# Kernel optimization log

Measured on AMD Instinct MI355X. Metric: run time of the kernel, lower is better.

Reference implementation:

```python
import jax, jax.numpy as jnp
import numpy as np

B, S_SRC, S_TRG = 128, 512, 128
VIN, VOUT = 128, 128
E, H = 128, 256          # embed, encoder hidden
HD = 2 * H               # decoder hidden = 512 (concat of bi-dir encoder states)
DENC = 2 * H             # encoder output feature dim = 512


def setup_inputs() -> dict:
    key = jax.random.key(0)
    ks = jax.random.split(key, 20)
    g = lambda k, shape: (jax.random.normal(k, shape, jnp.float32) * 0.05)
    inp = {
        "src": jax.random.randint(ks[0], (B, S_SRC), 0, VIN, jnp.int32),
        "trg": jax.random.randint(ks[1], (B, S_TRG), 0, VOUT, jnp.int32),
        # encoder
        "enc_emb": g(ks[2], (VIN, E)),
        "enc_Wih_f": g(ks[3], (4 * H, E)),
        "enc_Whh_f": g(ks[4], (4 * H, H)),
        "enc_b_f": g(ks[5], (4 * H,)),
        "enc_Wih_b": g(ks[6], (4 * H, E)),
        "enc_Whh_b": g(ks[7], (4 * H, H)),
        "enc_b_b": g(ks[8], (4 * H,)),
        # decoder
        "dec_emb": g(ks[9], (VOUT, E)),
        "dec_Wih": g(ks[10], (4 * HD, E + DENC)),
        "dec_Whh": g(ks[11], (4 * HD, HD)),
        "dec_b": g(ks[12], (4 * HD,)),
        # attention: Linear(dec_hid + enc_dim -> HD), v: Linear(HD -> 1)
        "attn_W": g(ks[13], (HD + DENC, HD)),
        "attn_b": g(ks[14], (HD,)),
        "attn_v": g(ks[15], (HD,)),
        # output projection
        "out_W": g(ks[16], (HD, VOUT)),
        "out_b": g(ks[17], (VOUT,)),
    }
    return inp


def _lstm_cell(h, c, x, Wih, Whh, b):
    gates = x @ Wih.T + h @ Whh.T + b               # [B, 4H]
    i, f, gg, o = jnp.split(gates, 4, axis=-1)       # PyTorch gate order i,f,g,o
    i, f, o = jax.nn.sigmoid(i), jax.nn.sigmoid(f), jax.nn.sigmoid(o)
    c = f * c + i * jnp.tanh(gg)
    h = o * jnp.tanh(c)
    return h, c


def _lstm_scan(xs, Wih, Whh, b, reverse=False):
    # xs: [S, B, E] -> hs: [S, B, H] (time-aligned), plus final (h, c)
    Bn, Hn = xs.shape[1], Whh.shape[1]
    init = (jnp.zeros((Bn, Hn), xs.dtype), jnp.zeros((Bn, Hn), xs.dtype))
    def step(carry, x):
        h, c = _lstm_cell(carry[0], carry[1], x, Wih, Whh, b)
        return (h, c), h
    (h, c), hs = jax.lax.scan(step, init, xs, reverse=reverse)
    return hs, h, c


def reference(src, trg, enc_emb, enc_Wih_f, enc_Whh_f, enc_b_f,
              enc_Wih_b, enc_Whh_b, enc_b_b, dec_emb, dec_Wih, dec_Whh,
              dec_b, attn_W, attn_b, attn_v, out_W, out_b):
    # ----- encoder (bidirectional LSTM) -----
    emb = enc_emb[src]                                # [B, S, E]
    xs = jnp.swapaxes(emb, 0, 1)                      # [S, B, E]
    hs_f, hf, cf = _lstm_scan(xs, enc_Wih_f, enc_Whh_f, enc_b_f, reverse=False)
    hs_b, hb, cb = _lstm_scan(xs, enc_Wih_b, enc_Whh_b, enc_b_b, reverse=True)
    enc_out = jnp.swapaxes(jnp.concatenate([hs_f, hs_b], -1), 0, 1)  # [B, S, 2H]
    hidden = jnp.concatenate([hf, hb], -1)            # [B, HD]  (hidden.view(1,B,-1))
    cell = jnp.concatenate([cf, cb], -1)              # [B, HD]

    # attention linear split: energy = tanh([h, enc] @ W + b)
    Wh, We = attn_W[:HD], attn_W[HD:]
    enc_proj = jnp.einsum("bsd,de->bse", enc_out, We)  # [B, S, HD] precomputed

    def dec_step(carry, tok):
        h, c = carry
        e = jnp.tanh(h[:, None, :] @ Wh + enc_proj + attn_b)     # [B, S, HD]
        scores = jnp.einsum("bse,e->bs", e, attn_v)              # [B, S]
        aw = jax.nn.softmax(scores, axis=1)
        ctx = jnp.einsum("bs,bsd->bd", aw, enc_out)              # [B, DENC]
        x = jnp.concatenate([dec_emb[tok], ctx], -1)             # [B, E+DENC]
        h, c = _lstm_cell(h, c, x, dec_Wih, dec_Whh, dec_b)
        logits = h @ out_W + out_b                               # [B, VOUT]
        return (h, c), logits

    # teacher forcing (ratio=1.0): input at step t is trg[:, t-1], t = 1..T-1
    toks = jnp.swapaxes(trg[:, :-1], 0, 1)            # [T-1, B]
    _, logits = jax.lax.scan(dec_step, (hidden, cell), toks)
    logits = jnp.swapaxes(logits, 0, 1)               # [B, T-1, VOUT]
    outputs = jnp.concatenate(
        [jnp.zeros((src.shape[0], 1, VOUT), logits.dtype), logits], axis=1)
    return outputs
```

## Files before the change

kernel.cpp:

```cpp
#include <hip/hip_runtime.h>


typedef _Float16 f16;
typedef _Float16 half8 __attribute__((ext_vector_type(8)));
typedef float f32x4 __attribute__((ext_vector_type(4)));
typedef char char8v __attribute__((ext_vector_type(8)));

#define MFMA16(a, b, c) __builtin_amdgcn_mfma_f32_16x16x32_f16((a), (b), (c), 0, 0, 0)

#define PSCALE (2.5f / 127.f)
#define PINV   (127.f / 2.5f)

__device__ __forceinline__ float fsig(float x) {
    return __builtin_amdgcn_rcpf(1.f + __expf(-x));
}
__device__ __forceinline__ float ftanh(float x) {
    return 1.f - 2.f * __builtin_amdgcn_rcpf(1.f + __expf(2.f * x));
}
__device__ __forceinline__ int frag_idx(int m, int k, int KS) {
    return (((m >> 4) * KS + (k >> 5)) * 64 + (((k >> 3) & 3) * 16 + (m & 15))) * 8 + (k & 7);
}

__global__ __launch_bounds__(256) void k_prep(
    const float* __restrict__ attn_W, const float* __restrict__ out_W,
    const float* __restrict__ enc_emb,
    const float* __restrict__ wihf, const float* __restrict__ wihb,
    const float* __restrict__ whhf, const float* __restrict__ whhb,
    const float* __restrict__ dec_emb, const float* __restrict__ dec_wih,
    const float* __restrict__ dec_whh,
    f16* __restrict__ WhT_sw, f16* __restrict__ outWT_sw,
    f16* __restrict__ whhf_sw, f16* __restrict__ whhb_sw,
    f16* __restrict__ decwih_sw, f16* __restrict__ decwhh_sw,
    f16* __restrict__ WeT, f16* __restrict__ emb16,
    f16* __restrict__ wihf16, f16* __restrict__ wihb16,
    f16* __restrict__ decemb16, float* __restrict__ out)
{
    long i = (long)blockIdx.x * 256 + threadIdx.x;
    if (i >= 3784704L) return;
    long idx = i;
    if (idx < 262144) {
        int j = idx & 7, lane = (idx >> 3) & 63, c = lane & 15, q = lane >> 4;
        int ks = (idx >> 9) & 15, nt = idx >> 13;
        WhT_sw[idx] = (f16)attn_W[(ks * 32 + q * 8 + j) * 512 + nt * 16 + c];
        return;
    }
    idx -= 262144;
    if (idx < 65536) {
        int j = idx & 7, lane = (idx >> 3) & 63, c = lane & 15, q = lane >> 4;
        int ks = (idx >> 9) & 15, nt = idx >> 13;
        outWT_sw[idx] = (f16)out_W[(ks * 32 + q * 8 + j) * 128 + nt * 16 + c];
        return;
    }
    idx -= 65536;
    if (idx < 262144) {
        int j = idx & 7, lane = (idx >> 3) & 63, c = lane & 15, q = lane >> 4;
        int ks = (idx >> 9) & 7, nt = idx >> 12;
        whhf_sw[idx] = (f16)whhf[(nt * 16 + c) * 256 + ks * 32 + q * 8 + j];
        return;
    }
    idx -= 262144;
    if (idx < 262144) {
        int j = idx & 7, lane = (idx >> 3) & 63, c = lane & 15, q = lane >> 4;
        int ks = (idx >> 9) & 7, nt = idx >> 12;
        whhb_sw[idx] = (f16)whhb[(nt * 16 + c) * 256 + ks * 32 + q * 8 + j];
        return;
    }
    idx -= 262144;
    if (idx < 1310720) {
        int j = idx & 7, lane = (idx >> 3) & 63, c = lane & 15, q = lane >> 4;
        int r2 = idx >> 9; int ks = r2 % 20, nt = r2 / 20;
        decwih_sw[idx] = (f16)dec_wih[(nt * 16 + c) * 640 + ks * 32 + q * 8 + j];
        return;
    }
    idx -= 1310720;
    if (idx < 1048576) {
        int j = idx & 7, lane = (idx >> 3) & 63, c = lane & 15, q = lane >> 4;
        int ks = (idx >> 9) & 15, nt = idx >> 13;
        decwhh_sw[idx] = (f16)dec_whh[(nt * 16 + c) * 512 + ks * 32 + q * 8 + j];
        return;
    }
    idx -= 1048576;
    if (idx < 262144) { int e = idx >> 9, d = idx & 511; WeT[idx] = (f16)attn_W[(512 + d) * 512 + e]; return; }
    idx -= 262144;
    if (idx < 16384)  { emb16[idx] = (f16)enc_emb[idx]; return; }
    idx -= 16384;
    if (idx < 131072) { wihf16[idx] = (f16)wihf[idx]; return; }
    idx -= 131072;
    if (idx < 131072) { wihb16[idx] = (f16)wihb[idx]; return; }
    idx -= 131072;
    if (idx < 16384)  { decemb16[idx] = (f16)dec_emb[idx]; return; }
    idx -= 16384;
    if (idx < 16384)  { int b = idx >> 7, v = idx & 127; out[b * 16384 + v] = 0.f; return; }
}

__global__ __launch_bounds__(256) void k_vocab(
    const f16* __restrict__ emb, const f16* __restrict__ wihf,
    const f16* __restrict__ wihb, const float* __restrict__ bf_,
    const float* __restrict__ bb_, f16* __restrict__ xg_vocab)
{
    int bn = blockIdx.x;
    int tid = threadIdx.x, wave = tid >> 6, lane = tid & 63;
    int col = lane & 15, quad = lane >> 4;
    int wr = wave >> 1, wc = wave & 1;

    f32x4 acc[4][4] = {};
    for (int ks = 0; ks < 4; ++ks) {
        int k0 = ks * 32 + quad * 8;
        half8 a[4], bfr[4];
        for (int i = 0; i < 4; ++i)
            a[i] = *(const half8*)(emb + (wr * 64 + i * 16 + col) * 128 + k0);
        for (int j = 0; j < 4; ++j) {
            int n = bn * 128 + wc * 64 + j * 16 + col;
            const f16* wp = (n < 1024) ? (wihf + n * 128) : (wihb + (n - 1024) * 128);
            bfr[j] = *(const half8*)(wp + k0);
        }
        for (int i = 0; i < 4; ++i)
            for (int j = 0; j < 4; ++j)
                acc[i][j] = MFMA16(a[i], bfr[j], acc[i][j]);
    }
    for (int j = 0; j < 4; ++j) {
        int n = bn * 128 + wc * 64 + j * 16 + col;
        float bias = (n < 1024) ? bf_[n] : bb_[n - 1024];
        for (int i = 0; i < 4; ++i) {
            int vbase = wr * 64 + i * 16 + quad * 4;
            for (int r = 0; r < 4; ++r)
                xg_vocab[(vbase + r) * 2048 + n] = (f16)(acc[i][j][r] + bias);
        }
    }
}

__global__ __launch_bounds__(512, 2) void k_enc(
    const int* __restrict__ src, const f16* __restrict__ xg_vocab,
    const f16* __restrict__ whhf_sw, const f16* __restrict__ whhb_sw,
    f16* __restrict__ enc_out, f16* __restrict__ hdec0, float* __restrict__ c_ws)
{
    int blk = blockIdx.x;
    int dir = blk >> 3, bbase = (blk & 7) * 16;
    int tid = threadIdx.x, wave = tid >> 6, lane = tid & 63;
    int col = lane & 15, quad = lane >> 4;
    const f16* whh = dir ? whhb_sw : whhf_sw;

    __shared__ f16 hb[16][264];
    __shared__ f16 xvb[16][1032];
    __shared__ int stok[16];
    for (int z = tid; z < 16 * 264; z += 512) ((f16*)hb)[z] = (f16)0.f;
    float cc[2][4] = {};

    half8 bst[32];
    #pragma unroll
    for (int g = 0; g < 2; ++g)
        #pragma unroll
        for (int nt = 0; nt < 2; ++nt)
            #pragma unroll
            for (int kk = 0; kk < 8; ++kk) {
                int tile = g * 16 + wave * 2 + nt;
                bst[(g * 2 + nt) * 8 + kk] =
                    *(const half8*)(whh + ((tile * 8 + kk) * 64 + lane) * 8);
            }
    __syncthreads();

    for (int t = 0; t < 512; ++t) {
        int ts = dir ? (511 - t) : t;
        if (tid < 16) stok[tid] = src[(bbase + tid) * 512 + ts];
        half8 a[8];
        #pragma unroll
        for (int kk = 0; kk < 8; ++kk)
            a[kk] = *(const half8*)(&hb[col][kk * 32 + quad * 8]);
        __syncthreads();

        #pragma unroll
        for (int it = 0; it < 4; ++it) {
            int cnk = it * 512 + tid;
            int row = cnk >> 7, off = (cnk & 127) * 8;
            *(half8*)(&xvb[row][off]) =
                *(const half8*)(xg_vocab + stok[row] * 2048 + dir * 1024 + off);
        }

        f32x4 acc[4][2] = {};
        #pragma unroll
        for (int kk = 0; kk < 8; ++kk) {
            half8 bv[4];
            #pragma unroll
            for (int g = 2; g < 4; ++g)
                #pragma unroll
                for (int nt = 0; nt < 2; ++nt) {
                    int tile = g * 16 + wave * 2 + nt;
                    bv[(g - 2) * 2 + nt] =
                        *(const half8*)(whh + ((tile * 8 + kk) * 64 + lane) * 8);
                }
            #pragma unroll
            for (int g = 0; g < 2; ++g)
                #pragma unroll
                for (int nt = 0; nt < 2; ++nt)
                    acc[g][nt] = MFMA16(a[kk], bst[(g * 2 + nt) * 8 + kk], acc[g][nt]);
            #pragma unroll
            for (int g = 2; g < 4; ++g)
                #pragma unroll
                for (int nt = 0; nt < 2; ++nt)
                    acc[g][nt] = MFMA16(a[kk], bv[(g - 2) * 2 + nt], acc[g][nt]);
        }
        __syncthreads();

        #pragma unroll
        for (int nt = 0; nt < 2; ++nt) {
            int hcol = wave * 32 + nt * 16 + col;
            #pragma unroll
            for (int r = 0; r < 4; ++r) {
                int b = quad * 4 + r;
                float gi = (float)xvb[b][0 * 256 + hcol] + acc[0][nt][r];
                float gf = (float)xvb[b][1 * 256 + hcol] + acc[1][nt][r];
                float gg = (float)xvb[b][2 * 256 + hcol] + acc[2][nt][r];
                float go = (float)xvb[b][3 * 256 + hcol] + acc[3][nt][r];
                float ig = fsig(gi), fg = fsig(gf), g2 = ftanh(gg), og = fsig(go);
                float cv = fg * cc[nt][r] + ig * g2;
                cc[nt][r] = cv;
                float h = og * ftanh(cv);
                f16 h16 = (f16)h;
                hb[b][hcol] = h16;
                enc_out[((size_t)(bbase + b) * 512 + ts) * 512 + dir * 256 + hcol] = h16;
            }
        }
        __syncthreads();
    }
    #pragma unroll
    for (int nt = 0; nt < 2; ++nt) {
        int hcol = wave * 32 + nt * 16 + col;
        #pragma unroll
        for (int r = 0; r < 4; ++r) {
            int b = quad * 4 + r;
            int m = bbase + b, k = dir * 256 + hcol;
            hdec0[frag_idx(m, k, 16)] = hb[b][hcol];
            c_ws[m * 512 + k] = cc[nt][r];
        }
    }
}

__global__ __launch_bounds__(256) void k_proj(
    const f16* __restrict__ enc_out, const f16* __restrict__ WeT,
    char* __restrict__ proj8)
{
    int blk = blockIdx.x;
    int bm = blk & 511, bn = blk >> 9;
    int tid = threadIdx.x, wave = tid >> 6, lane = tid & 63;
    int col = lane & 15, quad = lane >> 4;
    int wr = wave >> 1, wc = wave & 1;

    f32x4 acc[4][4] = {};
    for (int ks = 0; ks < 16; ++ks) {
        int k0 = ks * 32 + quad * 8;
        half8 a[4], bfr[4];
        for (int i = 0; i < 4; ++i) {
            int m = bm * 128 + wr * 64 + i * 16 + col;
            a[i] = *(const half8*)(enc_out + (size_t)m * 512 + k0);
        }
        for (int j = 0; j < 4; ++j) {
            int n = bn * 128 + wc * 64 + j * 16 + col;
            bfr[j] = *(const half8*)(WeT + n * 512 + k0);
        }
        for (int i = 0; i < 4; ++i)
            for (int j = 0; j < 4; ++j)
                acc[i][j] = MFMA16(a[i], bfr[j], acc[i][j]);
    }
    for (int j = 0; j < 4; ++j) {
        int n = bn * 128 + wc * 64 + j * 16 + col;
        for (int i = 0; i < 4; ++i) {
            int mbase = bm * 128 + wr * 64 + i * 16 + quad * 4;
            for (int r = 0; r < 4; ++r) {
                float v = acc[i][j][r] * PINV;
                int q = (int)rintf(v);
                q = (q > 127) ? 127 : ((q < -127) ? -127 : q);
                proj8[(size_t)(mbase + r) * 512 + n] = (char)q;
            }
        }
    }
}

__global__ __launch_bounds__(256) void k_qinit(
    const f16* __restrict__ h0_sw, const f16* __restrict__ WhT_sw,
    float* __restrict__ qpart)
{
    int j = blockIdx.x;
    int tid = threadIdx.x, wave = tid >> 6, lane = tid & 63;
    int col = lane & 15, quad = lane >> 4;
    half8 a[2];
    #pragma unroll
    for (int i = 0; i < 2; ++i)
        a[i] = *(const half8*)(h0_sw + (((wave * 2 + i) * 16 + j) * 64 + lane) * 8);
    for (int nt = 0; nt < 32; ++nt) {
        half8 bfr = *(const half8*)(WhT_sw + ((nt * 16 + j) * 64 + lane) * 8);
        f32x4 q0 = {}, q1 = {};
        q0 = MFMA16(a[0], bfr, q0);
        q1 = MFMA16(a[1], bfr, q1);
        #pragma unroll
        for (int r = 0; r < 4; ++r) {
            qpart[(j * 128 + wave * 32 + quad * 4 + r) * 512 + nt * 16 + col] = q0[r];
            qpart[(j * 128 + wave * 32 + 16 + quad * 4 + r) * 512 + nt * 16 + col] = q1[r];
        }
    }
}

__global__ __launch_bounds__(512) void k_att(
    const char* __restrict__ proj8, const f16* __restrict__ enc_out,
    const float* __restrict__ qpart, const float* __restrict__ attn_b,
    const float* __restrict__ attn_v, const int* __restrict__ trg,
    const f16* __restrict__ dec_emb, f16* __restrict__ x_sw,
    float* __restrict__ part_m, float* __restrict__ part_l,
    float* __restrict__ part_ctx, int t)
{
    int blk = blockIdx.x;
    int b = blk >> 1, sh = blk & 1;
    int tid = threadIdx.x, wave = tid >> 6, lane = tid & 63;
    __shared__ float q[512];
    __shared__ float sc[256];
    __shared__ float ctxred[8][512];
    __shared__ float wred[8], wred2[8];

    {
        float s = attn_b[tid];
        #pragma unroll
        for (int jj = 0; jj < 16; ++jj) s += qpart[(jj * 128 + b) * 512 + tid];
        q[tid] = s;
    }
    __syncthreads();

    float qreg[8], vreg[8];
    #pragma unroll
    for (int u = 0; u < 8; ++u) {
        int e = lane * 8 + u;
        qreg[u] = q[e];
        vreg[u] = attn_v[e];
    }
    int sbase = sh * 256;
    for (int ib = 0; ib < 4; ++ib) {
        char8v p[8];
        #pragma unroll
        for (int z = 0; z < 8; ++z) {
            int sl = (ib * 8 + z) * 8 + wave;
            p[z] = *(const char8v*)(proj8 + ((size_t)b * 512 + sbase + sl) * 512 + lane * 8);
        }
        #pragma unroll
        for (int z = 0; z < 8; ++z) {
            int sl = (ib * 8 + z) * 8 + wave;
            float part = 0.f;
            #pragma unroll
            for (int u = 0; u < 8; ++u)
                part += vreg[u] * ftanh(fmaf((float)p[z][u], PSCALE, qreg[u]));
            #pragma unroll
            for (int o = 32; o; o >>= 1) part += __shfl_xor(part, o);
            if (lane == 0) sc[sl] = part;
        }
    }
    __syncthreads();

    float s0 = (tid < 256) ? sc[tid] : -__builtin_inff();
    float mv = s0;
    #pragma unroll
    for (int o = 32; o; o >>= 1) mv = fmaxf(mv, __shfl_xor(mv, o));
    if (lane == 0) wred[wave] = mv;
    __syncthreads();
    float M = wred[0];
    #pragma unroll
    for (int w = 1; w < 8; ++w) M = fmaxf(M, wred[w]);
    float e0 = (tid < 256) ? __expf(s0 - M) : 0.f;
    if (tid < 256) sc[tid] = e0;
    float sm = e0;
    #pragma unroll
    for (int o = 32; o; o >>= 1) sm += __shfl_xor(sm, o);
    if (lane == 0) wred2[wave] = sm;
    __syncthreads();
    float lb = wred2[0];
    #pragma unroll
    for (int w = 1; w < 8; ++w) lb += wred2[w];

    float a8[8] = {};
    for (int ib = 0; ib < 4; ++ib) {
        half8 ev[8];
        float wgt[8];
        #pragma unroll
        for (int z = 0; z < 8; ++z) {
            int sl = (ib * 8 + z) * 8 + wave;
            ev[z] = *(const half8*)(enc_out + ((size_t)b * 512 + sbase + sl) * 512 + lane * 8);
            wgt[z] = sc[sl];
        }
        #pragma unroll
        for (int z = 0; z < 8; ++z)
            #pragma unroll
            for (int u = 0; u < 8; ++u) a8[u] += wgt[z] * (float)ev[z][u];
    }
    #pragma unroll
    for (int u = 0; u < 8; ++u) ctxred[wave][lane * 8 + u] = a8[u];
    __syncthreads();
    float cp = 0.f;
    #pragma unroll
    for (int w = 0; w < 8; ++w) cp += ctxred[w][tid];
    part_ctx[(size_t)blk * 512 + tid] = cp;
    if (tid == 0) { part_m[blk] = M; part_l[blk] = lb; }

    if (sh == 0 && tid < 128) {
        int tok = trg[b * 128 + t];
        x_sw[frag_idx(b, tid, 20)] = dec_emb[tok * 128 + tid];
    }
}

__global__ __launch_bounds__(256) void k_gates(
    f16* __restrict__ x_sw, const f16* __restrict__ hprev_sw,
    const f16* __restrict__ wih_sw, const f16* __restrict__ whh_sw,
    const float* __restrict__ dec_b, float* __restrict__ c_ws,
    f16* __restrict__ hnext_sw, f16* __restrict__ hhist_sw,
    const f16* __restrict__ WhT_sw, float* __restrict__ qpart,
    const float* __restrict__ part_m, const float* __restrict__ part_l,
    const float* __restrict__ part_ctx, int t)
{
    int jb = blockIdx.x;
    int j = jb >> 1, mh = jb & 1;
    int tid = threadIdx.x, wave = tid >> 6, lane = tid & 63;
    int col = lane & 15, quad = lane >> 4;
    __shared__ f16 hsl[64][40];
    __shared__ float gm[64][2];

    if (tid < 64) {
        int bb = mh * 64 + tid;
        float m0 = part_m[bb * 2 + 0], m1 = part_m[bb * 2 + 1];
        float l0 = part_l[bb * 2 + 0], l1 = part_l[bb * 2 + 1];
        float M = fmaxf(m0, m1);
        float g0 = __expf(m0 - M), g1 = __expf(m1 - M);
        float inv = 1.f / (g0 * l0 + g1 * l1);
        gm[tid][0] = g0 * inv;
        gm[tid][1] = g1 * inv;
    }
    __syncthreads();
    for (int z = tid; z < 32768; z += 256) {
        int lr = z >> 9, d = z & 511;
        int bb = mh * 64 + lr;
        float c = gm[lr][0] * part_ctx[(size_t)(bb * 2 + 0) * 512 + d]
                + gm[lr][1] * part_ctx[(size_t)(bb * 2 + 1) * 512 + d];
        x_sw[frag_idx(bb, 128 + d, 20)] = (f16)c;
    }
    __syncthreads();

    f32x4 acc[8] = {};
    for (int ks = 0; ks < 36; ++ks) {
        int mtile = mh * 4 + wave;
        half8 a = (ks < 20)
            ? *(const half8*)(x_sw + ((mtile * 20 + ks) * 64 + lane) * 8)
            : *(const half8*)(hprev_sw + ((mtile * 16 + (ks - 20)) * 64 + lane) * 8);
        half8 bv[8];
        #pragma unroll
        for (int jt = 0; jt < 8; ++jt) {
            int g = jt >> 1, u2 = jt & 1;
            int ntile = g * 32 + j * 2 + u2;
            bv[jt] = (ks < 20)
                ? *(const half8*)(wih_sw + ((ntile * 20 + ks) * 64 + lane) * 8)
                : *(const half8*)(whh_sw + ((ntile * 16 + (ks - 20)) * 64 + lane) * 8);
        }
        #pragma unroll
        for (int jt = 0; jt < 8; ++jt)
            acc[jt] = MFMA16(a, bv[jt], acc[jt]);
    }
    float bias[8];
    #pragma unroll
    for (int jt = 0; jt < 8; ++jt) {
        int g = jt >> 1, u2 = jt & 1;
        bias[jt] = dec_b[g * 512 + j * 32 + u2 * 16 + col];
    }
    #pragma unroll
    for (int r = 0; r < 4; ++r) {
        int lb = wave * 16 + quad * 4 + r;
        int bb = mh * 64 + lb;
        #pragma unroll
        for (int u2 = 0; u2 < 2; ++u2) {
            int hl = u2 * 16 + col, hcol = j * 32 + hl;
            float gi = acc[0 + u2][r] + bias[0 + u2];
            float gf = acc[2 + u2][r] + bias[2 + u2];
            float gg = acc[4 + u2][r] + bias[4 + u2];
            float go = acc[6 + u2][r] + bias[6 + u2];
            float ig = fsig(gi), fg = fsig(gf), g2 = ftanh(gg), og = fsig(go);
            float cv = fg * c_ws[bb * 512 + hcol] + ig * g2;
            c_ws[bb * 512 + hcol] = cv;
            float h = og * ftanh(cv);
            f16 h16 = (f16)h;
            int fidx = frag_idx(bb, hcol, 16);
            hnext_sw[fidx] = h16;
            hhist_sw[t * 65536 + fidx] = h16;
            hsl[lb][hl] = h16;
        }
    }
    half8 aq = *(const half8*)(&hsl[wave * 16 + col][quad * 8]);
    for (int nt = 0; nt < 32; ++nt) {
        half8 bq = *(const half8*)(WhT_sw + ((nt * 16 + j) * 64 + lane) * 8);
        f32x4 q0 = {};
        q0 = MFMA16(aq, bq, q0);
        #pragma unroll
        for (int r = 0; r < 4; ++r)
            qpart[(j * 128 + mh * 64 + wave * 16 + quad * 4 + r) * 512 + nt * 16 + col] = q0[r];
    }
}

__global__ __launch_bounds__(256) void k_logits(
    const f16* __restrict__ hhist_sw, const f16* __restrict__ outWT_sw,
    const float* __restrict__ out_b, float* __restrict__ out)
{
    int bt = blockIdx.x;
    int tid = threadIdx.x, wave = tid >> 6, lane = tid & 63;
    int col = lane & 15, quad = lane >> 4;
    f32x4 acc[2][8] = {};
    for (int ks = 0; ks < 16; ++ks) {
        half8 a[2];
        #pragma unroll
        for (int i = 0; i < 2; ++i)
            a[i] = *(const half8*)(hhist_sw + bt * 65536 + (((wave * 2 + i) * 16 + ks) * 64 + lane) * 8);
        half8 bv[8];
        #pragma unroll
        for (int jt = 0; jt < 8; ++jt)
            bv[jt] = *(const half8*)(outWT_sw + ((jt * 16 + ks) * 64 + lane) * 8);
        #pragma unroll
        for (int jt = 0; jt < 8; ++jt) {
            acc[0][jt] = MFMA16(a[0], bv[jt], acc[0][jt]);
            acc[1][jt] = MFMA16(a[1], bv[jt], acc[1][jt]);
        }
    }
    #pragma unroll
    for (int jt = 0; jt < 8; ++jt) {
        float bias = out_b[jt * 16 + col];
        #pragma unroll
        for (int i = 0; i < 2; ++i)
            #pragma unroll
            for (int r = 0; r < 4; ++r) {
                int br = wave * 32 + i * 16 + quad * 4 + r;
                out[br * 16384 + (bt + 1) * 128 + jt * 16 + col] = acc[i][jt][r] + bias;
            }
    }
}

extern "C" void kernel_launch(void* const* d_in, const int* in_sizes, int n_in,
                              void* d_out, int out_size, void* d_ws, size_t ws_size,
                              hipStream_t stream)
{
    (void)in_sizes; (void)n_in; (void)out_size;
    if (ws_size < 130000000) return;

    const int*   src     = (const int*)d_in[0];
    const int*   trg     = (const int*)d_in[1];
    const float* enc_emb = (const float*)d_in[2];
    const float* wihf    = (const float*)d_in[3];
    const float* whhf    = (const float*)d_in[4];
    const float* bf_     = (const float*)d_in[5];
    const float* wihb    = (const float*)d_in[6];
    const float* whhb    = (const float*)d_in[7];
    const float* bb_     = (const float*)d_in[8];
    const float* dec_emb = (const float*)d_in[9];
    const float* dec_wih = (const float*)d_in[10];
    const float* dec_whh = (const float*)d_in[11];
    const float* dec_b   = (const float*)d_in[12];
    const float* attn_W  = (const float*)d_in[13];
    const float* attn_b  = (const float*)d_in[14];
    const float* attn_v  = (const float*)d_in[15];
    const float* out_W   = (const float*)d_in[16];
    const float* out_b   = (const float*)d_in[17];
    float* out = (float*)d_out;

    char* p = (char*)d_ws;
    auto carve = [&](size_t n) { char* r = p; p += ((n + 255) & ~(size_t)255); return r; };
    f16*   enc_out   = (f16*)  carve(67108864);
    char*  proj8     = (char*) carve(33554432);
    f16*   WhT_sw    = (f16*)  carve(524288);
    f16*   WeT       = (f16*)  carve(524288);
    f16*   outWT_sw  = (f16*)  carve(131072);
    f16*   emb16     = (f16*)  carve(32768);
    f16*   wihf16    = (f16*)  carve(262144);
    f16*   wihb16    = (f16*)  carve(262144);
    f16*   whhf_sw   = (f16*)  carve(524288);
    f16*   whhb_sw   = (f16*)  carve(524288);
    f16*   decemb16  = (f16*)  carve(32768);
    f16*   decwih_sw = (f16*)  carve(2621440);
    f16*   decwhh_sw = (f16*)  carve(2097152);
    float* qpart     = (float*)carve(4194304);
    f16*   hdec0     = (f16*)  carve(131072);
    f16*   hdec1     = (f16*)  carve(131072);
    float* c_ws      = (float*)carve(262144);
    f16*   x_sw      = (f16*)  carve(163840);
    f16*   hhist_sw  = (f16*)  carve(16646144);
    f16*   xg_vocab  = (f16*)  carve(524288);
    float* part_m    = (float*)carve(2048);
    float* part_l    = (float*)carve(2048);
    float* part_ctx  = (float*)carve(524288);

    k_prep<<<14784, 256, 0, stream>>>(attn_W, out_W, enc_emb, wihf, wihb, whhf, whhb,
                                      dec_emb, dec_wih, dec_whh,
                                      WhT_sw, outWT_sw, whhf_sw, whhb_sw,
                                      decwih_sw, decwhh_sw, WeT, emb16,
                                      wihf16, wihb16, decemb16, out);
    k_vocab<<<16, 256, 0, stream>>>(emb16, wihf16, wihb16, bf_, bb_, xg_vocab);
    k_enc<<<16, 512, 0, stream>>>(src, xg_vocab, whhf_sw, whhb_sw, enc_out, hdec0, c_ws);
    k_proj<<<2048, 256, 0, stream>>>(enc_out, WeT, proj8);
    k_qinit<<<16, 256, 0, stream>>>(hdec0, WhT_sw, qpart);
    for (int t = 0; t < 127; ++t) {
        k_att<<<256, 512, 0, stream>>>(proj8, enc_out, qpart, attn_b, attn_v,
                                       trg, decemb16, x_sw, part_m, part_l,
                                       part_ctx, t);
        f16* hin  = (t & 1) ? hdec1 : hdec0;
        f16* hout = (t & 1) ? hdec0 : hdec1;
        k_gates<<<32, 256, 0, stream>>>(x_sw, hin, decwih_sw, decwhh_sw, dec_b,
                                        c_ws, hout, hhist_sw, WhT_sw, qpart,
                                        part_m, part_l, part_ctx, t);
    }
    k_logits<<<127, 256, 0, stream>>>(hhist_sw, outWT_sw, out_b, out);
}
```

Baseline: 13.05 ms.

## Fuse decoder time loop into one persistent cooperative kernel with grid syncs

Replaces the 254 per-step launches of the attention and gate kernels with a single cooperative kernel that loops over all 127 decoder steps and uses grid-wide barriers between the attention phase and the LSTM gate phase. This removes kernel launch overhead and launch gaps across the sequential decode. In exchange, only 16 of 256 blocks do the gate work while the rest idle at the barrier, and grid.sync cost is paid twice per step. The old multi-launch path remains as a fallback if the cooperative launch fails.

```diff
diff --git a/kernel.cpp b/kernel.cpp
--- a/kernel.cpp
+++ b/kernel.cpp
@@ -1,4 +1,7 @@
 #include <hip/hip_runtime.h>
+#include <hip/hip_cooperative_groups.h>
+
+namespace cg = cooperative_groups;
 
 
 typedef _Float16 f16;
@@ -493,6 +496,204 @@
         #pragma unroll
         for (int r = 0; r < 4; ++r)
             qpart[(j * 128 + mh * 64 + wave * 16 + quad * 4 + r) * 512 + nt * 16 + col] = q0[r];
+    }
+}
+
+__global__ __launch_bounds__(512, 2) void k_decode(
+    const char* __restrict__ proj8, const f16* __restrict__ enc_out,
+    float* __restrict__ qpart, const float* __restrict__ attn_bp,
+    const float* __restrict__ attn_vp, const int* __restrict__ trg,
+    const f16* __restrict__ dec_emb, f16* __restrict__ x_sw,
+    float* __restrict__ part_m, float* __restrict__ part_l,
+    float* __restrict__ part_ctx, f16* __restrict__ hdec0,
+    f16* __restrict__ hdec1, const f16* __restrict__ wih_sw,
+    const f16* __restrict__ whh_sw, const float* __restrict__ dec_bp,
+    float* __restrict__ c_ws, f16* __restrict__ hhist_sw,
+    const f16* __restrict__ WhT_sw)
+{
+    cg::grid_group grid = cg::this_grid();
+    int blk = blockIdx.x;
+    int tid = threadIdx.x, wave = tid >> 6, lane = tid & 63;
+    int col = lane & 15, quad = lane >> 4;
+    int b = blk >> 1, sh = blk & 1;
+    int sbase = sh * 256;
+
+    __shared__ float q[512];
+    __shared__ float sc[256];
+    __shared__ float ctxred[8][512];
+    __shared__ float wred[8], wred2[8];
+    __shared__ f16 hsl[128][40];
+    __shared__ float gm[128][2];
+
+    float vreg[8];
+    #pragma unroll
+    for (int u = 0; u < 8; ++u) vreg[u] = attn_vp[lane * 8 + u];
+    float ab = attn_bp[tid];
+
+    for (int t = 0; t < 127; ++t) {
+        {
+            float s = ab;
+            #pragma unroll
+            for (int jj = 0; jj < 16; ++jj) s += qpart[(jj * 128 + b) * 512 + tid];
+            q[tid] = s;
+        }
+        __syncthreads();
+        float qreg[8];
+        #pragma unroll
+        for (int u = 0; u < 8; ++u) qreg[u] = q[lane * 8 + u];
+
+        for (int ib = 0; ib < 4; ++ib) {
+            char8v p[8];
+            #pragma unroll
+            for (int z = 0; z < 8; ++z) {
+                int sl = (ib * 8 + z) * 8 + wave;
+                p[z] = *(const char8v*)(proj8 + ((size_t)b * 512 + sbase + sl) * 512 + lane * 8);
+            }
+            #pragma unroll
+            for (int z = 0; z < 8; ++z) {
+                int sl = (ib * 8 + z) * 8 + wave;
+                float part = 0.f;
+                #pragma unroll
+                for (int u = 0; u < 8; ++u)
+                    part += vreg[u] * ftanh(fmaf((float)p[z][u], PSCALE, qreg[u]));
+                #pragma unroll
+                for (int o = 32; o; o >>= 1) part += __shfl_xor(part, o);
+                if (lane == 0) sc[sl] = part;
+            }
+        }
+        __syncthreads();
+
+        float s0 = (tid < 256) ? sc[tid] : -__builtin_inff();
+        float mv = s0;
+        #pragma unroll
+        for (int o = 32; o; o >>= 1) mv = fmaxf(mv, __shfl_xor(mv, o));
+        if (lane == 0) wred[wave] = mv;
+        __syncthreads();
+        float M = wred[0];
+        #pragma unroll
+        for (int w = 1; w < 8; ++w) M = fmaxf(M, wred[w]);
+        float e0 = (tid < 256) ? __expf(s0 - M) : 0.f;
+        if (tid < 256) sc[tid] = e0;
+        float sm = e0;
+        #pragma unroll
+        for (int o = 32; o; o >>= 1) sm += __shfl_xor(sm, o);
+        if (lane == 0) wred2[wave] = sm;
+        __syncthreads();
+        float lsum = wred2[0];
+        #pragma unroll
+        for (int w = 1; w < 8; ++w) lsum += wred2[w];
+
+        float a8[8] = {};
+        for (int ib = 0; ib < 4; ++ib) {
+            half8 ev[8];
+            float wgt[8];
+            #pragma unroll
+            for (int z = 0; z < 8; ++z) {
+                int sl = (ib * 8 + z) * 8 + wave;
+                ev[z] = *(const half8*)(enc_out + ((size_t)b * 512 + sbase + sl) * 512 + lane * 8);
+                wgt[z] = sc[sl];
+            }
+            #pragma unroll
+            for (int z = 0; z < 8; ++z)
+                #pragma unroll
+                for (int u = 0; u < 8; ++u) a8[u] += wgt[z] * (float)ev[z][u];
+        }
+        #pragma unroll
+        for (int u = 0; u < 8; ++u) ctxred[wave][lane * 8 + u] = a8[u];
+        __syncthreads();
+        float cp = 0.f;
+        #pragma unroll
+        for (int w = 0; w < 8; ++w) cp += ctxred[w][tid];
+        part_ctx[(size_t)blk * 512 + tid] = cp;
+        if (tid == 0) { part_m[blk] = M; part_l[blk] = lsum; }
+
+        if (sh == 0 && tid < 128) {
+            int tok = trg[b * 128 + t];
+            x_sw[frag_idx(b, tid, 20)] = dec_emb[tok * 128 + tid];
+        }
+
+        grid.sync();
+
+        if (blk < 16) {
+            int j = blk;
+            if (tid < 128) {
+                float m0 = part_m[tid * 2 + 0], m1 = part_m[tid * 2 + 1];
+                float l0 = part_l[tid * 2 + 0], l1 = part_l[tid * 2 + 1];
+                float Mx = fmaxf(m0, m1);
+                float g0 = __expf(m0 - Mx), g1 = __expf(m1 - Mx);
+                float inv = 1.f / (g0 * l0 + g1 * l1);
+                gm[tid][0] = g0 * inv;
+                gm[tid][1] = g1 * inv;
+            }
+            __syncthreads();
+            for (int z = tid; z < 65536; z += 512) {
+                int lr = z >> 9, d = z & 511;
+                float cval = gm[lr][0] * part_ctx[(size_t)(lr * 2 + 0) * 512 + d]
+                           + gm[lr][1] * part_ctx[(size_t)(lr * 2 + 1) * 512 + d];
+                x_sw[frag_idx(lr, 128 + d, 20)] = (f16)cval;
+            }
+            __syncthreads();
+
+            const f16* hprev = (t & 1) ? hdec1 : hdec0;
+            f16* hnext = (t & 1) ? hdec0 : hdec1;
+
+            f32x4 acc[8] = {};
+            for (int ks = 0; ks < 36; ++ks) {
+                half8 a = (ks < 20)
+                    ? *(const half8*)(x_sw + ((wave * 20 + ks) * 64 + lane) * 8)
+                    : *(const half8*)(hprev + ((wave * 16 + (ks - 20)) * 64 + lane) * 8);
+                half8 bv[8];
+                #pragma unroll
+                for (int jt = 0; jt < 8; ++jt) {
+                    int g = jt >> 1, u2 = jt & 1;
+                    int ntile = g * 32 + j * 2 + u2;
+                    bv[jt] = (ks < 20)
+                        ? *(const half8*)(wih_sw + ((ntile * 20 + ks) * 64 + lane) * 8)
+                        : *(const half8*)(whh_sw + ((ntile * 16 + (ks - 20)) * 64 + lane) * 8);
+                }
+                #pragma unroll
+                for (int jt = 0; jt < 8; ++jt)
+                    acc[jt] = MFMA16(a, bv[jt], acc[jt]);
+            }
+            float bias[8];
+            #pragma unroll
+            for (int jt = 0; jt < 8; ++jt) {
+                int g = jt >> 1, u2 = jt & 1;
+                bias[jt] = dec_bp[g * 512 + j * 32 + u2 * 16 + col];
+            }
+            #pragma unroll
+            for (int r = 0; r < 4; ++r) {
+                int bb = wave * 16 + quad * 4 + r;
+                #pragma unroll
+                for (int u2 = 0; u2 < 2; ++u2) {
+                    int hl = u2 * 16 + col, hcol = j * 32 + hl;
+                    float gi = acc[0 + u2][r] + bias[0 + u2];
+                    float gf = acc[2 + u2][r] + bias[2 + u2];
+                    float gg = acc[4 + u2][r] + bias[4 + u2];
+                    float go = acc[6 + u2][r] + bias[6 + u2];
+                    float ig = fsig(gi), fg = fsig(gf), g2 = ftanh(gg), og = fsig(go);
+                    float cv = fg * c_ws[bb * 512 + hcol] + ig * g2;
+                    c_ws[bb * 512 + hcol] = cv;
+                    float h = og * ftanh(cv);
+                    f16 h16 = (f16)h;
+                    int fidx = frag_idx(bb, hcol, 16);
+                    hnext[fidx] = h16;
+                    hhist_sw[t * 65536 + fidx] = h16;
+                    hsl[bb][hl] = h16;
+                }
+            }
+            half8 aq = *(const half8*)(&hsl[wave * 16 + col][quad * 8]);
+            for (int nt = 0; nt < 32; ++nt) {
+                half8 bq = *(const half8*)(WhT_sw + ((nt * 16 + j) * 64 + lane) * 8);
+                f32x4 q0 = {};
+                q0 = MFMA16(aq, bq, q0);
+                #pragma unroll
+                for (int r = 0; r < 4; ++r)
+                    qpart[(j * 128 + wave * 16 + quad * 4 + r) * 512 + nt * 16 + col] = q0[r];
+            }
+        }
+
+        grid.sync();
     }
 }
 
@@ -594,15 +795,41 @@
     k_enc<<<16, 512, 0, stream>>>(src, xg_vocab, whhf_sw, whhb_sw, enc_out, hdec0, c_ws);
     k_proj<<<2048, 256, 0, stream>>>(enc_out, WeT, proj8);
     k_qinit<<<16, 256, 0, stream>>>(hdec0, WhT_sw, qpart);
-    for (int t = 0; t < 127; ++t) {
-        k_att<<<256, 512, 0, stream>>>(proj8, enc_out, qpart, attn_b, attn_v,
-                                       trg, decemb16, x_sw, part_m, part_l,
-                                       part_ctx, t);
-        f16* hin  = (t & 1) ? hdec1 : hdec0;
-        f16* hout = (t & 1) ? hdec0 : hdec1;
-        k_gates<<<32, 256, 0, stream>>>(x_sw, hin, decwih_sw, decwhh_sw, dec_b,
-                                        c_ws, hout, hhist_sw, WhT_sw, qpart,
-                                        part_m, part_l, part_ctx, t);
-    }
+
+    void* dargs[19];
+    dargs[0]  = (void*)&proj8;
+    dargs[1]  = (void*)&enc_out;
+    dargs[2]  = (void*)&qpart;
+    dargs[3]  = (void*)&attn_b;
+    dargs[4]  = (void*)&attn_v;
+    dargs[5]  = (void*)&trg;
+    dargs[6]  = (void*)&decemb16;
+    dargs[7]  = (void*)&x_sw;
+    dargs[8]  = (void*)&part_m;
+    dargs[9]  = (void*)&part_l;
+    dargs[10] = (void*)&part_ctx;
+    dargs[11] = (void*)&hdec0;
+    dargs[12] = (void*)&hdec1;
+    dargs[13] = (void*)&decwih_sw;
+    dargs[14] = (void*)&decwhh_sw;
+    dargs[15] = (void*)&dec_b;
+    dargs[16] = (void*)&c_ws;
+    dargs[17] = (void*)&hhist_sw;
+    dargs[18] = (void*)&WhT_sw;
+    hipError_t ce = hipLaunchCooperativeKernel(k_decode, dim3(256), dim3(512),
+                                               dargs, 0u, stream);
+    if (ce != hipSuccess) {
+        for (int t = 0; t < 127; ++t) {
+            k_att<<<256, 512, 0, stream>>>(proj8, enc_out, qpart, attn_b, attn_v,
+                                           trg, decemb16, x_sw, part_m, part_l,
+                                           part_ctx, t);
+            f16* hin  = (t & 1) ? hdec1 : hdec0;
+            f16* hout = (t & 1) ? hdec0 : hdec1;
+            k_gates<<<32, 256, 0, stream>>>(x_sw, hin, decwih_sw, decwhh_sw, dec_b,
+                                            c_ws, hout, hhist_sw, WhT_sw, qpart,
+                                            part_m, part_l, part_ctx, t);
+        }
+    }
+
     k_logits<<<127, 256, 0, stream>>>(hhist_sw, outWT_sw, out_b, out);
 }
```

Measured after the change: 25.57 ms. +96.0%, slower.

## Prefetch encoder tokens and gate inputs one step ahead, vectorize output stores

Applied to the files above, without the earlier changes.

The encoder recurrence now preloads all source tokens for its batch slice into shared memory and prefetches the next timestep's vocabulary gate rows into registers while the current step's MFMAs run. Scattered per-element enc_out stores are replaced by coalesced 16-byte stores from shared memory, deferred to the next iteration, which also removes one barrier per step. Launch bounds drop to one block per SM to give registers room for the prefetch buffers, at the cost of occupancy and a large 32KB shared token array.

```diff
diff --git a/kernel.cpp b/kernel.cpp
--- a/kernel.cpp
+++ b/kernel.cpp
@@ -129,7 +129,7 @@
     }
 }
 
-__global__ __launch_bounds__(512, 2) void k_enc(
+__global__ __launch_bounds__(512, 1) void k_enc(
     const int* __restrict__ src, const f16* __restrict__ xg_vocab,
     const f16* __restrict__ whhf_sw, const f16* __restrict__ whhb_sw,
     f16* __restrict__ enc_out, f16* __restrict__ hdec0, float* __restrict__ c_ws)
@@ -142,8 +142,10 @@
 
     __shared__ f16 hb[16][264];
     __shared__ f16 xvb[16][1032];
-    __shared__ int stok[16];
+    __shared__ int stall[8192];
+
     for (int z = tid; z < 16 * 264; z += 512) ((f16*)hb)[z] = (f16)0.f;
+    for (int z = tid; z < 8192; z += 512) stall[z] = src[bbase * 512 + z];
     float cc[2][4] = {};
 
     half8 bst[32];
@@ -159,21 +161,44 @@
             }
     __syncthreads();
 
+    int xrow = tid >> 7, xoff = (tid & 127) * 8;
+    half8 xr[4];
+    {
+        int ts0 = dir ? 511 : 0;
+        #pragma unroll
+        for (int it = 0; it < 4; ++it) {
+            int row = it * 4 + xrow;
+            int tok = stall[row * 512 + ts0];
+            xr[it] = *(const half8*)(xg_vocab + tok * 2048 + dir * 1024 + xoff);
+        }
+    }
+
+    int ts_prev = 0;
     for (int t = 0; t < 512; ++t) {
         int ts = dir ? (511 - t) : t;
-        if (tid < 16) stok[tid] = src[(bbase + tid) * 512 + ts];
+
+        if (t > 0) {
+            int b = tid >> 5, seg = tid & 31;
+            *(half8*)(enc_out + ((size_t)(bbase + b) * 512 + ts_prev) * 512 + dir * 256 + seg * 8) =
+                *(const half8*)(&hb[b][seg * 8]);
+        }
+        #pragma unroll
+        for (int it = 0; it < 4; ++it)
+            *(half8*)(&xvb[it * 4 + xrow][xoff]) = xr[it];
         half8 a[8];
         #pragma unroll
         for (int kk = 0; kk < 8; ++kk)
             a[kk] = *(const half8*)(&hb[col][kk * 32 + quad * 8]);
         __syncthreads();
 
-        #pragma unroll
-        for (int it = 0; it < 4; ++it) {
-            int cnk = it * 512 + tid;
-            int row = cnk >> 7, off = (cnk & 127) * 8;
-            *(half8*)(&xvb[row][off]) =
-                *(const half8*)(xg_vocab + stok[row] * 2048 + dir * 1024 + off);
+        if (t < 511) {
+            int tsn = dir ? (510 - t) : (t + 1);
+            #pragma unroll
+            for (int it = 0; it < 4; ++it) {
+                int row = it * 4 + xrow;
+                int tok = stall[row * 512 + tsn];
+                xr[it] = *(const half8*)(xg_vocab + tok * 2048 + dir * 1024 + xoff);
+            }
         }
 
         f32x4 acc[4][2] = {};
@@ -199,7 +224,6 @@
                 for (int nt = 0; nt < 2; ++nt)
                     acc[g][nt] = MFMA16(a[kk], bv[(g - 2) * 2 + nt], acc[g][nt]);
         }
-        __syncthreads();
 
         #pragma unroll
         for (int nt = 0; nt < 2; ++nt) {
@@ -215,12 +239,17 @@
                 float cv = fg * cc[nt][r] + ig * g2;
                 cc[nt][r] = cv;
                 float h = og * ftanh(cv);
-                f16 h16 = (f16)h;
-                hb[b][hcol] = h16;
-                enc_out[((size_t)(bbase + b) * 512 + ts) * 512 + dir * 256 + hcol] = h16;
+                hb[b][hcol] = (f16)h;
             }
         }
         __syncthreads();
+        ts_prev = ts;
+    }
+
+    {
+        int b = tid >> 5, seg = tid & 31;
+        *(half8*)(enc_out + ((size_t)(bbase + b) * 512 + ts_prev) * 512 + dir * 256 + seg * 8) =
+            *(const half8*)(&hb[b][seg * 8]);
     }
     #pragma unroll
     for (int nt = 0; nt < 2; ++nt) {
```

New measurement: 13.39 ms. 1.03x slower.
